# Performance work log

Measured on AMD Instinct MI355X. Metric: run time of the kernel, lower is better.

The kernel has to match this reference:

```python
import jax, jax.numpy as jnp
import numpy as np
import math

B, C, H, W = 16, 256, 128, 128
N = 4096
D = 256  # out_channels
IMG = 512


def _bilinear_sample(features, grid):
    """features (B,C,H,W), grid (B,N,2) in [-1,1] (x,y). align_corners=True, border padding."""
    Bq, Cq, Hq, Wq = features.shape
    ix = (grid[..., 0] + 1.0) * 0.5 * (Wq - 1)  # (B,N)
    iy = (grid[..., 1] + 1.0) * 0.5 * (Hq - 1)
    # border padding: clamp continuous coords into valid range
    ix = jnp.clip(ix, 0.0, Wq - 1)
    iy = jnp.clip(iy, 0.0, Hq - 1)
    x0 = jnp.floor(ix)
    y0 = jnp.floor(iy)
    wx = ix - x0
    wy = iy - y0
    x0i = jnp.clip(x0.astype(jnp.int32), 0, Wq - 1)
    y0i = jnp.clip(y0.astype(jnp.int32), 0, Hq - 1)
    x1i = jnp.clip(x0i + 1, 0, Wq - 1)
    y1i = jnp.clip(y0i + 1, 0, Hq - 1)
    f = features.reshape(Bq, Cq, Hq * Wq)

    def gather(yi, xi):
        idx = (yi * Wq + xi)[:, None, :]  # (B,1,N)
        return jnp.take_along_axis(f, idx, axis=2)  # (B,C,N)

    v00 = gather(y0i, x0i)
    v01 = gather(y0i, x1i)
    v10 = gather(y1i, x0i)
    v11 = gather(y1i, x1i)
    wx = wx[:, None, :]
    wy = wy[:, None, :]
    top = v00 * (1 - wx) + v01 * wx
    bot = v10 * (1 - wx) + v11 * wx
    return top * (1 - wy) + bot * wy  # (B,C,N)


def _pos_encoding(positions, d_model):
    """positions (B,N,2) in [0,1] -> (B,N,2*d_model) sinusoidal."""
    div_term = jnp.exp(jnp.arange(0, d_model, 2, dtype=jnp.float32)
                       * (-math.log(10000.0) / d_model))  # (d_model//2,)
    x = positions[..., 0:1] * 1000.0  # (B,N,1)
    y = positions[..., 1:2] * 1000.0

    def interleave(v):
        a = v * div_term  # (B,N,d_model//2)
        sc = jnp.stack([jnp.sin(a), jnp.cos(a)], axis=-1)  # (B,N,d//2,2)
        return sc.reshape(*v.shape[:-1], d_model)

    return jnp.concatenate([interleave(x), interleave(y)], axis=-1)


def setup_inputs() -> dict:
    key = jax.random.key(0)
    ks = jax.random.split(key, 8)
    features = jax.random.normal(ks[0], (B, C, H, W), dtype=jnp.float32)
    vertices = jax.random.uniform(ks[1], (B, N, 2), dtype=jnp.float32) * IMG
    s1 = 1.0 / math.sqrt(C)
    s2 = 1.0 / math.sqrt(D)
    W1 = jax.random.uniform(ks[2], (C, D), jnp.float32, -s1, s1)
    b1 = jnp.zeros((D,), jnp.float32)
    W2 = jax.random.uniform(ks[3], (D, D), jnp.float32, -s2, s2)
    b2 = jnp.zeros((D,), jnp.float32)
    Wp = jax.random.uniform(ks[4], (D, D), jnp.float32, -s2, s2)
    bp = jnp.zeros((D,), jnp.float32)
    return {"features": features, "vertices": vertices, "image_size": IMG,
            "W1": W1, "b1": b1, "W2": W2, "b2": b2, "Wp": Wp, "bp": bp}


def reference(features, vertices, image_size, W1, b1, W2, b2, Wp, bp):
    # normalize pixel coords to [-1,1] (align_corners=True convention)
    denom = jnp.float32(image_size - 1)
    grid = 2.0 * vertices / denom - 1.0  # (B,N,2)
    sampled = _bilinear_sample(features, grid)  # (B,C,N)
    sampled = jnp.transpose(sampled, (0, 2, 1))  # (B,N,C)
    h = jax.nn.relu(jnp.einsum('bnc,cd->bnd', sampled, W1) + b1)
    vfeat = jnp.einsum('bnd,de->bne', h, W2) + b2  # (B,N,D)
    pos_enc = _pos_encoding(vertices / jnp.float32(image_size), D // 2)  # (B,N,D)
    out = jnp.einsum('bnd,de->bne', vfeat + pos_enc, Wp) + bp
    return out
```

## Files before the change

### kernel.cpp

```cpp
#include <hip/hip_runtime.h>

#define HW 16384
#define Nn 4096

typedef __bf16 bf16x8 __attribute__((ext_vector_type(8)));
typedef unsigned short us8t __attribute__((ext_vector_type(8)));
typedef float f32x4 __attribute__((ext_vector_type(4)));
typedef float f32x16 __attribute__((ext_vector_type(16)));

__device__ __forceinline__ unsigned short f2bf(float f) {
    unsigned int u = __float_as_uint(f);
    u = (u + 0x7fffu + ((u >> 16) & 1u)) >> 16;
    return (unsigned short)u;
}
__device__ __forceinline__ float bf2f(unsigned int h) {
    return __uint_as_float(h << 16);
}
__device__ __forceinline__ f32x4 mfma16(us8t a, us8t b, f32x4 c) {
    return __builtin_amdgcn_mfma_f32_16x16x32_bf16(
        __builtin_bit_cast(bf16x8, a), __builtin_bit_cast(bf16x8, b), c, 0, 0, 0);
}
__device__ __forceinline__ f32x16 mfma32(us8t a, us8t b, f32x16 c) {
    return __builtin_amdgcn_mfma_f32_32x32x16_bf16(
        __builtin_bit_cast(bf16x8, a), __builtin_bit_cast(bf16x8, b), c, 0, 0, 0);
}

__device__ __forceinline__ void gload16(const float* g, float* l) {
    __builtin_amdgcn_global_load_lds(
        (const __attribute__((address_space(1))) unsigned int*)g,
        (__attribute__((address_space(3))) unsigned int*)l, 16, 0, 0);
}

__global__ __launch_bounds__(256) void k_wt(const float* __restrict__ W1,
                                            const float* __restrict__ W2,
                                            const float* __restrict__ Wp,
                                            unsigned short* __restrict__ WT) {
    const int m = blockIdx.x >> 8;
    const int d = blockIdx.x & 255;
    const int c = threadIdx.x;
    const float* W = (m == 0) ? W1 : (m == 1) ? W2 : Wp;
    WT[m * 65536 + d * 256 + c] = f2bf(W[c * 256 + d]);
}

__global__ __launch_bounds__(512, 2) void k_gemm1(const float* __restrict__ f,
                                                  const unsigned short* __restrict__ W1T,
                                                  unsigned short* __restrict__ S, int b0) {
    __shared__ __align__(16) float fs[2][64][256];

    int blk = blockIdx.x;
    if ((gridDim.x & 7) == 0) {
        const int chunk = gridDim.x >> 3;
        blk = (blk & 7) * chunk + (blk >> 3);
    }
    const int bl = blk >> 6;
    const int b = b0 + bl;
    const int p0 = (blk & 63) << 8;
    const int t = threadIdx.x;
    const int lane = t & 63;
    const int w = t >> 6;
    const int l5 = lane >> 5;
    const int r31 = lane & 31;
    const int wp = w & 3;
    const int wd = w >> 2;

    const float* fb = f + ((size_t)b << 22) + p0;

    f32x16 acc[2][4];
#pragma unroll
    for (int i = 0; i < 2; ++i)
#pragma unroll
        for (int j = 0; j < 4; ++j)
#pragma unroll
            for (int r = 0; r < 16; ++r) acc[i][j][r] = 0.f;

    auto stage = [&](int bufi, int kt) {
#pragma unroll
        for (int i = 0; i < 8; ++i) {
            const int c = (w << 3) + i;
            gload16(fb + ((size_t)(((kt) << 6) + c) << 14) + (lane << 2), &fs[bufi][c][0]);
        }
    };

    stage(0, 0);
    __syncthreads();

    const int plA = (wp << 6) + r31;

    for (int kt = 0; kt < 4; ++kt) {
        const int cur = kt & 1;
        if (kt < 3) stage(cur ^ 1, kt + 1);

#pragma unroll
        for (int h = 0; h < 4; ++h) {
            const int cb = (h << 4) + (l5 << 3);
            us8t A[2];
#pragma unroll
            for (int mt = 0; mt < 2; ++mt) {
                const int pl = plA + (mt << 5);
                float av[8];
#pragma unroll
                for (int j = 0; j < 8; ++j) av[j] = fs[cur][cb + j][pl];
#pragma unroll
                for (int j = 0; j < 8; ++j) A[mt][j] = f2bf(av[j]);
            }
#pragma unroll
            for (int nt = 0; nt < 4; ++nt) {
                const int col = (wd << 7) + (nt << 5) + r31;
                const us8t bfr = *(const us8t*)(W1T + (col << 8) + (kt << 6) + cb);
                acc[0][nt] = mfma32(A[0], bfr, acc[0][nt]);
                acc[1][nt] = mfma32(A[1], bfr, acc[1][nt]);
            }
        }
        __syncthreads();
    }

    unsigned short* Sp = S + ((((size_t)bl << 14) + p0) << 8);
    const int rbase = l5 << 2;
#pragma unroll
    for (int mt = 0; mt < 2; ++mt)
#pragma unroll
        for (int nt = 0; nt < 4; ++nt) {
            const int d = (wd << 7) + (nt << 5) + r31;
#pragma unroll
            for (int r = 0; r < 16; ++r) {
                const int row = (wp << 6) + (mt << 5) + ((r >> 2) << 3) + (r & 3) + rbase;
                Sp[((size_t)row << 8) + d] = f2bf(acc[mt][nt][r]);
            }
        }
}

__global__ __launch_bounds__(256) void k_fused(const unsigned short* __restrict__ S,
                                               const float* __restrict__ verts,
                                               const int* __restrict__ iszp,
                                               const unsigned short* __restrict__ W2T,
                                               const unsigned short* __restrict__ WpT,
                                               const float* __restrict__ b1,
                                               const float* __restrict__ b2,
                                               const float* __restrict__ bpv,
                                               float* __restrict__ out, int b0) {
    __shared__ __align__(16) unsigned short hT[64][264];
    __shared__ __align__(16) int pIdx[64][4];
    __shared__ __align__(16) float wBl[64][4];
    __shared__ float vps[64][2];
    __shared__ __align__(16) float b1s[256];
    __shared__ float b2s[256], bps[256];

    const int blk = blockIdx.x;
    const int bl = blk >> 6;
    const int b = b0 + bl;
    const int n0 = (blk & 63) << 6;
    const int t = threadIdx.x;
    const int lane = t & 63;
    const int w = t >> 6;

    b1s[t] = b1[t];
    b2s[t] = b2[t];
    bps[t] = bpv[t];

    if (t < 64) {
        const float isz = (float)iszp[0];
        const size_t vo = ((size_t)b * Nn + n0 + t) << 1;
        const float vx = verts[vo + 0];
        const float vy = verts[vo + 1];
        const float gs = 127.0f / (isz - 1.0f);
        const float ix = fminf(fmaxf(vx * gs, 0.0f), 127.0f);
        const float iy = fminf(fmaxf(vy * gs, 0.0f), 127.0f);
        const float x0 = floorf(ix), y0 = floorf(iy);
        const float wx = ix - x0, wy = iy - y0;
        const int x0i = (int)x0, y0i = (int)y0;
        const int x1i = min(x0i + 1, 127), y1i = min(y0i + 1, 127);
        pIdx[t][0] = (y0i << 7) + x0i;
        pIdx[t][1] = (y0i << 7) + x1i;
        pIdx[t][2] = (y1i << 7) + x0i;
        pIdx[t][3] = (y1i << 7) + x1i;
        wBl[t][0] = (1.0f - wx) * (1.0f - wy);
        wBl[t][1] = wx * (1.0f - wy);
        wBl[t][2] = (1.0f - wx) * wy;
        wBl[t][3] = wx * wy;
        vps[t][0] = vx / isz;
        vps[t][1] = vy / isz;
    }
    __syncthreads();

    {
        const unsigned short* Sb = S + ((size_t)bl << 22);
        const float4 bl1 = *(const float4*)&b1s[lane << 2];
        for (int i = 0; i < 16; ++i) {
            const int r = (w << 4) + i;
            const int4 pp = *(const int4*)pIdx[r];
            const float4 wt = *(const float4*)wBl[r];
            const uint2 a0 = *(const uint2*)(Sb + ((size_t)pp.x << 8) + (lane << 2));
            const uint2 a1 = *(const uint2*)(Sb + ((size_t)pp.y << 8) + (lane << 2));
            const uint2 a2 = *(const uint2*)(Sb + ((size_t)pp.z << 8) + (lane << 2));
            const uint2 a3 = *(const uint2*)(Sb + ((size_t)pp.w << 8) + (lane << 2));
            float d0 = wt.x * bf2f(a0.x & 0xffffu) + wt.y * bf2f(a1.x & 0xffffu) +
                       wt.z * bf2f(a2.x & 0xffffu) + wt.w * bf2f(a3.x & 0xffffu) + bl1.x;
            float d1 = wt.x * bf2f(a0.x >> 16) + wt.y * bf2f(a1.x >> 16) +
                       wt.z * bf2f(a2.x >> 16) + wt.w * bf2f(a3.x >> 16) + bl1.y;
            float d2 = wt.x * bf2f(a0.y & 0xffffu) + wt.y * bf2f(a1.y & 0xffffu) +
                       wt.z * bf2f(a2.y & 0xffffu) + wt.w * bf2f(a3.y & 0xffffu) + bl1.z;
            float d3 = wt.x * bf2f(a0.y >> 16) + wt.y * bf2f(a1.y >> 16) +
                       wt.z * bf2f(a2.y >> 16) + wt.w * bf2f(a3.y >> 16) + bl1.w;
            d0 = fmaxf(d0, 0.0f);
            d1 = fmaxf(d1, 0.0f);
            d2 = fmaxf(d2, 0.0f);
            d3 = fmaxf(d3, 0.0f);
            uint2 pk;
            pk.x = (unsigned)f2bf(d0) | ((unsigned)f2bf(d1) << 16);
            pk.y = (unsigned)f2bf(d2) | ((unsigned)f2bf(d3) << 16);
            *(uint2*)&hT[r][lane << 2] = pk;
        }
    }
    __syncthreads();

    const int mrow = lane & 15;
    const int kg = (lane >> 4) << 3;
    const int r0 = (lane >> 4) << 2;
    const int n0w = w << 6;

    f32x4 acc[4][4];
#pragma unroll
    for (int i = 0; i < 4; ++i)
#pragma unroll
        for (int j = 0; j < 4; ++j) acc[i][j] = (f32x4){0.f, 0.f, 0.f, 0.f};

    us8t bnx[4];
#pragma unroll
    for (int nt = 0; nt < 4; ++nt)
        bnx[nt] = *(const us8t*)(W2T + ((n0w + (nt << 4) + mrow) << 8) + kg);
    for (int k0 = 0; k0 < 256; k0 += 32) {
        us8t bcur[4];
#pragma unroll
        for (int nt = 0; nt < 4; ++nt) bcur[nt] = bnx[nt];
        if (k0 < 224) {
#pragma unroll
            for (int nt = 0; nt < 4; ++nt)
                bnx[nt] = *(const us8t*)(W2T + ((n0w + (nt << 4) + mrow) << 8) + k0 + 32 + kg);
        }
        us8t af[4];
#pragma unroll
        for (int mt = 0; mt < 4; ++mt)
            af[mt] = *(const us8t*)&hT[(mt << 4) + mrow][k0 + kg];
#pragma unroll
        for (int mt = 0; mt < 4; ++mt)
#pragma unroll
            for (int nt = 0; nt < 4; ++nt)
                acc[mt][nt] = mfma16(af[mt], bcur[nt], acc[mt][nt]);
    }
    __syncthreads();

    const float C2 = -0.20762050593046f;
#pragma unroll
    for (int nt = 0; nt < 4; ++nt) {
        const int col = n0w + (nt << 4) + mrow;
        const float bias2 = b2s[col];
        const int ci = col & 127;
        const float dv = exp2f((float)(ci >> 1) * C2) * 1000.0f;
        const int sel = col >> 7;
#pragma unroll
        for (int mt = 0; mt < 4; ++mt)
#pragma unroll
            for (int j = 0; j < 4; ++j) {
                const int row = (mt << 4) + r0 + j;
                const float ang = vps[row][sel] * dv;
                const float pe = (col & 1) ? __cosf(ang) : __sinf(ang);
                hT[row][col] = f2bf(acc[mt][nt][j] + bias2 + pe);
            }
    }
    __syncthreads();

#pragma unroll
    for (int i = 0; i < 4; ++i)
#pragma unroll
        for (int j = 0; j < 4; ++j) acc[i][j] = (f32x4){0.f, 0.f, 0.f, 0.f};
#pragma unroll
    for (int nt = 0; nt < 4; ++nt)
        bnx[nt] = *(const us8t*)(WpT + ((n0w + (nt << 4) + mrow) << 8) + kg);
    for (int k0 = 0; k0 < 256; k0 += 32) {
        us8t bcur[4];
#pragma unroll
        for (int nt = 0; nt < 4; ++nt) bcur[nt] = bnx[nt];
        if (k0 < 224) {
#pragma unroll
            for (int nt = 0; nt < 4; ++nt)
                bnx[nt] = *(const us8t*)(WpT + ((n0w + (nt << 4) + mrow) << 8) + k0 + 32 + kg);
        }
        us8t af[4];
#pragma unroll
        for (int mt = 0; mt < 4; ++mt)
            af[mt] = *(const us8t*)&hT[(mt << 4) + mrow][k0 + kg];
#pragma unroll
        for (int mt = 0; mt < 4; ++mt)
#pragma unroll
            for (int nt = 0; nt < 4; ++nt)
                acc[mt][nt] = mfma16(af[mt], bcur[nt], acc[mt][nt]);
    }

    float* ob = out + (((size_t)b * Nn + n0) << 8);
#pragma unroll
    for (int nt = 0; nt < 4; ++nt) {
        const int col = n0w + (nt << 4) + mrow;
        const float bb = bps[col];
#pragma unroll
        for (int mt = 0; mt < 4; ++mt)
#pragma unroll
            for (int j = 0; j < 4; ++j) {
                const int row = (mt << 4) + r0 + j;
                ob[((size_t)row << 8) + col] = acc[mt][nt][j] + bb;
            }
    }
}

extern "C" void kernel_launch(void* const* d_in, const int* in_sizes, int n_in,
                              void* d_out, int out_size, void* d_ws, size_t ws_size,
                              hipStream_t stream) {
    const float* f = (const float*)d_in[0];
    const float* verts = (const float*)d_in[1];
    const int* isz = (const int*)d_in[2];
    const float* W1 = (const float*)d_in[3];
    const float* b1 = (const float*)d_in[4];
    const float* W2 = (const float*)d_in[5];
    const float* b2 = (const float*)d_in[6];
    const float* Wp = (const float*)d_in[7];
    const float* bp = (const float*)d_in[8];
    float* out = (float*)d_out;

    unsigned short* WT = (unsigned short*)d_ws;
    const size_t S_OFF = 512u << 10;
    unsigned short* S = (unsigned short*)((char*)d_ws + S_OFF);

    const size_t perBatch = (size_t)HW * 256 * 2;
    size_t sbytes = (ws_size > S_OFF) ? (ws_size - S_OFF) : 0;
    int nbMax = (int)(sbytes / perBatch);
    if (nbMax < 1) nbMax = 1;
    if (nbMax > 16) nbMax = 16;

    k_wt<<<dim3(768), dim3(256), 0, stream>>>(W1, W2, Wp, WT);
    for (int b0 = 0; b0 < 16; b0 += nbMax) {
        const int nb = (16 - b0 < nbMax) ? (16 - b0) : nbMax;
        k_gemm1<<<dim3(nb * 64), dim3(512), 0, stream>>>(f, WT, S, b0);
        k_fused<<<dim3(nb * 64), dim3(256), 0, stream>>>(S, verts, isz, WT + 65536, WT + 131072,
                                                         b1, b2, bp, out, b0);
    }
}
```

Baseline: 520.6 us.

## Split gemm1 output columns across four blocks with smaller K stages

```diff
diff --git a/kernel.cpp b/kernel.cpp
--- a/kernel.cpp
+++ b/kernel.cpp
@@ -42,75 +42,80 @@
     WT[m * 65536 + d * 256 + c] = f2bf(W[c * 256 + d]);
 }
 
-__global__ __launch_bounds__(512, 2) void k_gemm1(const float* __restrict__ f,
-                                                  const unsigned short* __restrict__ W1T,
-                                                  unsigned short* __restrict__ S, int b0) {
-    __shared__ __align__(16) float fs[2][64][256];
+__global__ __launch_bounds__(256) void k_gemm1(const float* __restrict__ f,
+                                               const unsigned short* __restrict__ W1T,
+                                               unsigned short* __restrict__ S, int b0) {
+    __shared__ __align__(16) float fs[2][16][256];
 
     int blk = blockIdx.x;
     if ((gridDim.x & 7) == 0) {
         const int chunk = gridDim.x >> 3;
         blk = (blk & 7) * chunk + (blk >> 3);
     }
-    const int bl = blk >> 6;
+    const int bl = blk >> 8;
     const int b = b0 + bl;
-    const int p0 = (blk & 63) << 8;
+    const int pt = (blk >> 2) & 63;
+    const int dt = blk & 2 ? (blk & 3) : (blk & 3);
+    const int p0 = pt << 8;
+    const int d0 = (blk & 3) << 6;
     const int t = threadIdx.x;
     const int lane = t & 63;
     const int w = t >> 6;
     const int l5 = lane >> 5;
     const int r31 = lane & 31;
-    const int wp = w & 3;
-    const int wd = w >> 2;
+    (void)dt;
 
     const float* fb = f + ((size_t)b << 22) + p0;
 
-    f32x16 acc[2][4];
+    f32x16 acc[2][2];
 #pragma unroll
     for (int i = 0; i < 2; ++i)
 #pragma unroll
-        for (int j = 0; j < 4; ++j)
+        for (int j = 0; j < 2; ++j)
 #pragma unroll
             for (int r = 0; r < 16; ++r) acc[i][j][r] = 0.f;
 
     auto stage = [&](int bufi, int kt) {
 #pragma unroll
-        for (int i = 0; i < 8; ++i) {
-            const int c = (w << 3) + i;
-            gload16(fb + ((size_t)(((kt) << 6) + c) << 14) + (lane << 2), &fs[bufi][c][0]);
+        for (int i = 0; i < 4; ++i) {
+            const int c = (w << 2) + i;
+            gload16(fb + ((size_t)((kt << 4) + c) << 14) + (lane << 2), &fs[bufi][c][0]);
         }
     };
 
     stage(0, 0);
     __syncthreads();
 
-    const int plA = (wp << 6) + r31;
-
-    for (int kt = 0; kt < 4; ++kt) {
+    const int plA = (w << 6) + r31;
+    const int cb = l5 << 3;
+
+    for (int kt = 0; kt < 16; ++kt) {
         const int cur = kt & 1;
-        if (kt < 3) stage(cur ^ 1, kt + 1);
-
-#pragma unroll
-        for (int h = 0; h < 4; ++h) {
-            const int cb = (h << 4) + (l5 << 3);
-            us8t A[2];
-#pragma unroll
-            for (int mt = 0; mt < 2; ++mt) {
-                const int pl = plA + (mt << 5);
-                float av[8];
-#pragma unroll
-                for (int j = 0; j < 8; ++j) av[j] = fs[cur][cb + j][pl];
-#pragma unroll
-                for (int j = 0; j < 8; ++j) A[mt][j] = f2bf(av[j]);
-            }
-#pragma unroll
-            for (int nt = 0; nt < 4; ++nt) {
-                const int col = (wd << 7) + (nt << 5) + r31;
-                const us8t bfr = *(const us8t*)(W1T + (col << 8) + (kt << 6) + cb);
-                acc[0][nt] = mfma32(A[0], bfr, acc[0][nt]);
-                acc[1][nt] = mfma32(A[1], bfr, acc[1][nt]);
-            }
-        }
+        if (kt < 15) stage(cur ^ 1, kt + 1);
+
+        us8t bfr[2];
+#pragma unroll
+        for (int nt = 0; nt < 2; ++nt) {
+            const int col = d0 + (nt << 5) + r31;
+            bfr[nt] = *(const us8t*)(W1T + (col << 8) + (kt << 4) + cb);
+        }
+
+        us8t A[2];
+#pragma unroll
+        for (int mt = 0; mt < 2; ++mt) {
+            const int pl = plA + (mt << 5);
+            float av[8];
+#pragma unroll
+            for (int j = 0; j < 8; ++j) av[j] = fs[cur][cb + j][pl];
+#pragma unroll
+            for (int j = 0; j < 8; ++j) A[mt][j] = f2bf(av[j]);
+        }
+#pragma unroll
+        for (int mt = 0; mt < 2; ++mt)
+#pragma unroll
+            for (int nt = 0; nt < 2; ++nt)
+                acc[mt][nt] = mfma32(A[mt], bfr[nt], acc[mt][nt]);
+
         __syncthreads();
     }
 
@@ -119,11 +124,11 @@
 #pragma unroll
     for (int mt = 0; mt < 2; ++mt)
 #pragma unroll
-        for (int nt = 0; nt < 4; ++nt) {
-            const int d = (wd << 7) + (nt << 5) + r31;
+        for (int nt = 0; nt < 2; ++nt) {
+            const int d = d0 + (nt << 5) + r31;
 #pragma unroll
             for (int r = 0; r < 16; ++r) {
-                const int row = (wp << 6) + (mt << 5) + ((r >> 2) << 3) + (r & 3) + rbase;
+                const int row = (w << 6) + (mt << 5) + ((r >> 2) << 3) + (r & 3) + rbase;
                 Sp[((size_t)row << 8) + d] = f2bf(acc[mt][nt][r]);
             }
         }
@@ -338,7 +343,7 @@
     k_wt<<<dim3(768), dim3(256), 0, stream>>>(W1, W2, Wp, WT);
     for (int b0 = 0; b0 < 16; b0 += nbMax) {
         const int nb = (16 - b0 < nbMax) ? (16 - b0) : nbMax;
-        k_gemm1<<<dim3(nb * 64), dim3(512), 0, stream>>>(f, WT, S, b0);
+        k_gemm1<<<dim3(nb * 256), dim3(256), 0, stream>>>(f, WT, S, b0);
         k_fused<<<dim3(nb * 64), dim3(256), 0, stream>>>(S, verts, isz, WT + 65536, WT + 131072,
                                                          b1, b2, bp, out, b0);
     }
```

Measured after the change: 533.0 us. 2.4% more time.
